# Performance work log

Measured on AMD Instinct MI355X. Metric: run time of the kernel, lower is better.

## Reference

```python
import jax, jax.numpy as jnp
import numpy as np

EMBED_DIM = 512
NUM_HEADS = 8
HEAD_DIM = EMBED_DIM // NUM_HEADS  # 64
ROT_T = 32  # head_dim * rope_fraction // 2
ROT_V = 32
ROPE_BASE = 10000.0


def _rope_cos_sin(idx, rot_dim, base=ROPE_BASE):
    # idx: (S,) int positions -> cos,sin: (S, rot_dim//2)
    half = rot_dim // 2
    inv_freq = 1.0 / (base ** (jnp.arange(half, dtype=jnp.float32) / half))
    angles = idx.astype(jnp.float32)[:, None] * inv_freq[None, :]  # (S, half)
    return jnp.cos(angles), jnp.sin(angles)


def _apply_rope(x, cos, sin):
    # x: (B,H,S,R) with R even; cos/sin: (S, R//2)
    xe = x[..., ::2]
    xo = x[..., 1::2]
    c = cos[None, None]  # (1,1,S,R//2)
    s = sin[None, None]
    oe = xe * c - xo * s
    oo = xe * s + xo * c
    # re-interleave even/odd lanes
    return jnp.stack([oe, oo], axis=-1).reshape(x.shape)


def setup_inputs() -> dict:
    key = jax.random.key(0)
    ks = jax.random.split(key, 5)
    B, S, D = 2, 4096, EMBED_DIM
    scale_w = 1.0 / np.sqrt(D)
    return {
        "x": jax.random.normal(ks[0], (B, S, D), dtype=jnp.float32),
        "Wq": jax.random.normal(ks[1], (D, D), dtype=jnp.float32) * scale_w,
        "Wk": jax.random.normal(ks[2], (D, D), dtype=jnp.float32) * scale_w,
        "Wv": jax.random.normal(ks[3], (D, D), dtype=jnp.float32) * scale_w,
        "Wo": jax.random.normal(ks[4], (D, D), dtype=jnp.float32) * scale_w,
        "T": 128,
        "V": 32,
    }


def reference(x, Wq, Wk, Wv, Wo, T, V):
    B, S, D = x.shape
    H, hd = NUM_HEADS, HEAD_DIM
    scale = hd ** -0.5

    def split_heads(y):
        return y.reshape(B, S, H, hd).transpose(0, 2, 1, 3)  # (B,H,S,hd)

    q = split_heads(x @ Wq.T)
    k = split_heads(x @ Wk.T)
    v = split_heads(x @ Wv.T)

    p = jnp.arange(S)
    t_idx = p // V
    v_idx = p % V
    cos_t, sin_t = _rope_cos_sin(t_idx, ROT_T)
    cos_v, sin_v = _rope_cos_sin(v_idx, ROT_V)

    te, ve = ROT_T, ROT_T + ROT_V
    q = jnp.concatenate([
        _apply_rope(q[..., :te], cos_t, sin_t),
        _apply_rope(q[..., te:ve], cos_v, sin_v),
        q[..., ve:],
    ], axis=-1)
    k = jnp.concatenate([
        _apply_rope(k[..., :te], cos_t, sin_t),
        _apply_rope(k[..., te:ve], cos_v, sin_v),
        k[..., ve:],
    ], axis=-1)

    attn = jnp.einsum("bhqd,bhkd->bhqk", q, k) * scale  # (B,H,S,S)
    attn = jax.nn.softmax(attn, axis=-1)
    y = jnp.einsum("bhqk,bhkd->bhqd", attn, v)
    y = y.transpose(0, 2, 1, 3).reshape(B, S, D)
    return y @ Wo.T
```

## Files before the change

kernel.cpp:

```cpp
#include <hip/hip_runtime.h>
#include <hip/hip_bf16.h>

#define SEQ 4096
#define BSZ 2
#define NH 8
#define HD 64
#define DMODEL 512

typedef __bf16 bf16_t;
typedef __bf16 bf16x8 __attribute__((ext_vector_type(8)));
typedef __bf16 bf16x4 __attribute__((ext_vector_type(4)));
typedef float f32x4 __attribute__((ext_vector_type(4)));

__device__ __forceinline__ f32x4 mfma16(bf16x8 a, bf16x8 b, f32x4 c) {
    return __builtin_amdgcn_mfma_f32_16x16x32_bf16(a, b, c, 0, 0, 0);
}

__device__ __forceinline__ bf16x8 ld8(const bf16_t* p) {
    return *reinterpret_cast<const bf16x8*>(p);
}

__device__ __forceinline__ uint32_t pack2(bf16_t a, bf16_t b) {
    union { bf16_t h[2]; uint32_t u; } x;
    x.h[0] = a; x.h[1] = b;
    return x.u;
}

__device__ __forceinline__ void gl_lds16(const bf16_t* g, bf16_t* l) {
    __builtin_amdgcn_global_load_lds(
        (const __attribute__((address_space(1))) uint32_t*)g,
        (__attribute__((address_space(3))) uint32_t*)l,
        16, 0, 0);
}

__global__ void cast_all(const float* __restrict__ x,
                         const float* __restrict__ wq, const float* __restrict__ wk,
                         const float* __restrict__ wv, const float* __restrict__ wo,
                         bf16_t* __restrict__ Xb, bf16_t* __restrict__ Wc,
                         bf16_t* __restrict__ Wob) {
    int i = blockIdx.x * blockDim.x + threadIdx.x;
    const float* src;
    bf16_t* dst;
    int j;
    if (i < 1048576) { src = x; dst = Xb; j = i; }
    else {
        int k = i - 1048576;
        int w = k >> 16;
        j = k & 65535;
        src = (w == 0) ? wq : (w == 1) ? wk : (w == 2) ? wv : wo;
        dst = (w == 3) ? Wob : Wc + w * 262144;
    }
    float4 v = reinterpret_cast<const float4*>(src)[j];
    bf16x4 o;
    o[0] = (bf16_t)v.x; o[1] = (bf16_t)v.y; o[2] = (bf16_t)v.z; o[3] = (bf16_t)v.w;
    reinterpret_cast<bf16x4*>(dst)[j] = o;
}

__global__ __launch_bounds__(256) void gemm_qkv(const bf16_t* __restrict__ A,
                                                const bf16_t* __restrict__ W,
                                                bf16_t* __restrict__ Qb,
                                                bf16_t* __restrict__ Kb,
                                                bf16_t* __restrict__ Vb,
                                                const int* __restrict__ Vpar) {
    __shared__ bf16_t As[2 * 128 * 32];
    __shared__ bf16_t Bs[2 * 128 * 32];
    const int lane = threadIdx.x & 63;
    const int wid = threadIdx.x >> 6;
    const int c = lane & 15, quad = lane >> 4;
    const int wm = wid & 1, wn = wid >> 1;
    const int m0 = blockIdx.x * 128;
    const int n0 = blockIdx.y * 128;

    f32x4 acc[4][4];
#pragma unroll
    for (int i = 0; i < 4; i++)
#pragma unroll
        for (int j = 0; j < 4; j++) acc[i][j] = f32x4{0.f, 0.f, 0.f, 0.f};

    const int lrow = lane >> 2;
    const int lch = lane & 3;
    const bf16_t* Ag = A + (size_t)(m0 + wid * 32 + lrow) * 512 + lch * 8;
    const bf16_t* Bg = W + (size_t)(n0 + wid * 32 + lrow) * 512 + lch * 8;
    const int w0 = (wid * 32) * 32;
    const int w1 = (wid * 32 + 16) * 32;

    gl_lds16(Ag, As + w0);
    gl_lds16(Ag + 16 * 512, As + w1);
    gl_lds16(Bg, Bs + w0);
    gl_lds16(Bg + 16 * 512, Bs + w1);

    for (int it = 0; it < 16; it++) {
        __syncthreads();

        if (it + 1 < 16) {
            int k0 = (it + 1) * 32;
            int bo = ((it + 1) & 1) * 4096;
            gl_lds16(Ag + k0, As + bo + w0);
            gl_lds16(Ag + 16 * 512 + k0, As + bo + w1);
            gl_lds16(Bg + k0, Bs + bo + w0);
            gl_lds16(Bg + 16 * 512 + k0, Bs + bo + w1);
        }

        const bf16_t* Ab = As + (it & 1) * 4096;
        const bf16_t* Bb = Bs + (it & 1) * 4096;
        bf16x8 a[4], b[4];
#pragma unroll
        for (int i = 0; i < 4; i++) a[i] = ld8(&Ab[(wm * 64 + i * 16 + c) * 32 + quad * 8]);
#pragma unroll
        for (int j = 0; j < 4; j++) b[j] = ld8(&Bb[(wn * 64 + j * 16 + c) * 32 + quad * 8]);
#pragma unroll
        for (int i = 0; i < 4; i++)
#pragma unroll
            for (int j = 0; j < 4; j++) acc[i][j] = mfma16(a[i], b[j], acc[i][j]);
    }

    const int Vv = Vpar[0];
    const float qs = 0.1803368801111204f;
    const bool codd = (c & 1);

#pragma unroll
    for (int i = 0; i < 4; i++) {
        int mbase = m0 + wm * 64 + i * 16 + quad * 4;
#pragma unroll
        for (int j = 0; j < 4; j++) {
            int col = n0 + wn * 64 + j * 16 + c;
            int which = col >> 9;
            int h = (col >> 6) & 7;
            int d = col & 63;
            f32x4 v = acc[i][j];
            if (which < 2) {
                int fidx = (d & 31) >> 1;
                float inv = exp2f((float)fidx * -0.8304820237218407f);
                bool hi = (d >= 32);
                f32x4 part;
#pragma unroll
                for (int r = 0; r < 4; r++) part[r] = __shfl_xor(v[r], 1, 64);
#pragma unroll
                for (int r = 0; r < 4; r++) {
                    int s = (mbase + r) & 4095;
                    int tq = s / Vv;
                    int vq = s - tq * Vv;
                    float ang = (float)(hi ? vq : tq) * inv;
                    float sn = __sinf(ang), cs = __cosf(ang);
                    float xe = codd ? part[r] : v[r];
                    float xo = codd ? v[r] : part[r];
                    v[r] = codd ? (xe * sn + xo * cs) : (xe * cs - xo * sn);
                }
                if (which == 0) {
#pragma unroll
                    for (int r = 0; r < 4; r++) v[r] *= qs;
                }
            }
            bf16_t* dst = (which == 0) ? Qb : ((which == 1) ? Kb : Vb);

            float p0 = __shfl_xor(v[0], 1, 64);
            float p1 = __shfl_xor(v[1], 1, 64);
            float p2 = __shfl_xor(v[2], 1, 64);
            float p3 = __shfl_xor(v[3], 1, 64);
            uint32_t u0 = codd ? pack2((bf16_t)p2, (bf16_t)v[2])
                               : pack2((bf16_t)v[0], (bf16_t)p0);
            uint32_t u1 = codd ? pack2((bf16_t)p3, (bf16_t)v[3])
                               : pack2((bf16_t)v[1], (bf16_t)p1);
            int dcol = d & ~1;
            int m = mbase + (codd ? 2 : 0);
            {
                int b_ = m >> 12, s = m & 4095;
                *(uint32_t*)&dst[((size_t)(b_ * NH + h) * SEQ + s) * HD + dcol] = u0;
                m++;
                b_ = m >> 12; s = m & 4095;
                *(uint32_t*)&dst[((size_t)(b_ * NH + h) * SEQ + s) * HD + dcol] = u1;
            }
        }
    }
}

__global__ __launch_bounds__(256) void gemm_out(const bf16_t* __restrict__ A,
                                                const bf16_t* __restrict__ W,
                                                float* __restrict__ out) {
    __shared__ bf16_t As[2 * 128 * 32];
    __shared__ bf16_t Bs[2 * 64 * 32];
    const int t = threadIdx.x;
    const int lane = t & 63;
    const int wid = t >> 6;
    const int c = lane & 15, quad = lane >> 4;
    const int m0 = blockIdx.x * 128;
    const int n0 = blockIdx.y * 64;

    f32x4 acc[2][4];
#pragma unroll
    for (int i = 0; i < 2; i++)
#pragma unroll
        for (int j = 0; j < 4; j++) acc[i][j] = f32x4{0.f, 0.f, 0.f, 0.f};

    const int lrow = lane >> 2;
    const int lch = lane & 3;
    const bf16_t* Ag = A + (size_t)(m0 + wid * 32 + lrow) * 512 + lch * 8;
    const bf16_t* Bg = W + (size_t)(n0 + wid * 16 + lrow) * 512 + lch * 8;
    const int aw0 = (wid * 32) * 32;
    const int aw1 = (wid * 32 + 16) * 32;
    const int bw = (wid * 16) * 32;

    gl_lds16(Ag, As + aw0);
    gl_lds16(Ag + 16 * 512, As + aw1);
    gl_lds16(Bg, Bs + bw);

    for (int it = 0; it < 16; it++) {
        __syncthreads();

        if (it + 1 < 16) {
            int k0 = (it + 1) * 32;
            int ao = ((it + 1) & 1) * 4096;
            int bo = ((it + 1) & 1) * 2048;
            gl_lds16(Ag + k0, As + ao + aw0);
            gl_lds16(Ag + 16 * 512 + k0, As + ao + aw1);
            gl_lds16(Bg + k0, Bs + bo + bw);
        }

        const bf16_t* Ab = As + (it & 1) * 4096;
        const bf16_t* Bb = Bs + (it & 1) * 2048;
        bf16x8 a[2], b[4];
#pragma unroll
        for (int i = 0; i < 2; i++) a[i] = ld8(&Ab[(wid * 32 + i * 16 + c) * 32 + quad * 8]);
#pragma unroll
        for (int j = 0; j < 4; j++) b[j] = ld8(&Bb[(j * 16 + c) * 32 + quad * 8]);
#pragma unroll
        for (int i = 0; i < 2; i++)
#pragma unroll
            for (int j = 0; j < 4; j++) acc[i][j] = mfma16(a[i], b[j], acc[i][j]);
    }

#pragma unroll
    for (int i = 0; i < 2; i++) {
        int mbase = m0 + wid * 32 + i * 16 + quad * 4;
#pragma unroll
        for (int j = 0; j < 4; j++) {
            int col = n0 + j * 16 + c;
#pragma unroll
            for (int r = 0; r < 4; r++)
                out[(size_t)(mbase + r) * DMODEL + col] = acc[i][j][r];
        }
    }
}

__global__ __launch_bounds__(256, 2) void flash_attn(const bf16_t* __restrict__ Q,
                                                     const bf16_t* __restrict__ K,
                                                     const bf16_t* __restrict__ V,
                                                     bf16_t* __restrict__ Y) {
    __shared__ __align__(16) unsigned char smem[65536];

    const int t = threadIdx.x;
    const int lane = t & 63;
    const int c = lane & 15, quad = lane >> 4;
    const int wid = t >> 6;
    const int w = wid & 1;
    const int pr = wid >> 1;
    const int bh = blockIdx.x & 15;
    const int qx = blockIdx.x >> 4;
    const int qw = qx * 128 + w * 64;

    size_t base = (size_t)bh * SEQ * HD;
    const bf16_t* Qp = Q + base;
    const bf16_t* Vp = V + base + (size_t)pr * 2048 * HD;

    unsigned char* pairBase = smem + pr * 32768;

    const bf16_t* Kpb = K + base + (size_t)pr * 2048 * HD;
    int srcOff = w * 4096 + ((lane >> 3) * 128) +
                 (((lane & 7) ^ ((lane >> 3) & 3)) * 16);
    const bf16_t* kE = (const bf16_t*)((const unsigned char*)Kpb + srcOff);
    const bf16_t* kO = (const bf16_t*)((const unsigned char*)Kpb + (srcOff ^ 64));

    bf16x8 qf[4][2];
#pragma unroll
    for (int qt = 0; qt < 4; qt++)
#pragma unroll
        for (int ks = 0; ks < 2; ks++)
            qf[qt][ks] = ld8(Qp + (size_t)(qw + qt * 16 + c) * HD + ks * 32 + quad * 8);

    f32x4 acc[4][4];
#pragma unroll
    for (int qt = 0; qt < 4; qt++)
#pragma unroll
        for (int dt = 0; dt < 4; dt++) acc[qt][dt] = f32x4{0.f, 0.f, 0.f, 0.f};
    float lsum[4] = {0.f, 0.f, 0.f, 0.f};

    const int tp = t & 127;
    const int kva = 2 * (tp & 31);
    const int dc = 16 * (tp >> 5);

    {
        bf16_t* dst = (bf16_t*)(pairBase + w * 4096);
#pragma unroll
        for (int i = 0; i < 4; i++)
            gl_lds16(((i & 1) ? kO : kE) + i * 512, dst + i * 512);
        kE += 4096; kO += 4096;
    }
    bf16x8 vr0 = ld8(Vp + (size_t)kva * HD + dc);
    bf16x8 vr1 = ld8(Vp + (size_t)(kva + 1) * HD + dc);
    bf16x8 vr2 = ld8(Vp + (size_t)kva * HD + dc + 8);
    bf16x8 vr3 = ld8(Vp + (size_t)(kva + 1) * HD + dc + 8);

    for (int kt = 0; kt < 32; kt++) {
        uint32_t* vt = (uint32_t*)(pairBase + 16384 + (kt & 1) * 8192);

#pragma unroll
        for (int j = 0; j < 8; j++) {
            int d0 = dc + j;
            int sv0 = (d0 & 7) ^ ((d0 >> 3) & 7);
            vt[d0 * 32 + (((kva >> 3) ^ sv0) & 7) * 4 + ((kva & 6) >> 1)] = pack2(vr0[j], vr1[j]);
            int d1 = dc + 8 + j;
            int sv1 = (d1 & 7) ^ ((d1 >> 3) & 7);
            vt[d1 * 32 + (((kva >> 3) ^ sv1) & 7) * 4 + ((kva & 6) >> 1)] = pack2(vr2[j], vr3[j]);
        }

        __syncthreads();

        if (kt + 1 < 32) {
            bf16_t* dst = (bf16_t*)(pairBase + ((kt + 1) & 1) * 8192 + w * 4096);
#pragma unroll
            for (int i = 0; i < 4; i++)
                gl_lds16(((i & 1) ? kO : kE) + i * 512, dst + i * 512);
            kE += 4096; kO += 4096;
            int kv0n = (kt + 1) * 64;
            vr0 = ld8(Vp + (size_t)(kv0n + kva) * HD + dc);
            vr1 = ld8(Vp + (size_t)(kv0n + kva + 1) * HD + dc);
            vr2 = ld8(Vp + (size_t)(kv0n + kva) * HD + dc + 8);
            vr3 = ld8(Vp + (size_t)(kv0n + kva + 1) * HD + dc + 8);
        }

        const uint4* kl = (const uint4*)(pairBase + (kt & 1) * 8192);

        f32x4 st[4][4];
#pragma unroll
        for (int n = 0; n < 4; n++) {
            int kvr = (n >> 1) * 32 + ((c >> 2) * 8) + ((n & 1) * 4) + (c & 3);
            int sk = (kvr & 3) | (((kvr >> 3) & 1) << 2);
            bf16x8 k0 = *reinterpret_cast<const bf16x8*>(&kl[kvr * 8 + (quad ^ sk)]);
            bf16x8 k1 = *reinterpret_cast<const bf16x8*>(&kl[kvr * 8 + ((4 + quad) ^ sk)]);
#pragma unroll
            for (int qt = 0; qt < 4; qt++) {
                f32x4 z = f32x4{0.f, 0.f, 0.f, 0.f};
                z = mfma16(k0, qf[qt][0], z);
                z = mfma16(k1, qf[qt][1], z);
                st[qt][n] = z;
            }
        }

        bf16x8 pf[4][2];
#pragma unroll
        for (int qt = 0; qt < 4; qt++) {
            float e[4][4];
            float ls = 0.f;
#pragma unroll
            for (int n = 0; n < 4; n++)
#pragma unroll
                for (int r = 0; r < 4; r++) {
                    float v = __builtin_amdgcn_exp2f(st[qt][n][r]);
                    e[n][r] = v;
                    ls += v;
                }
            lsum[qt] += ls;
            bf16x8 f0, f1;
#pragma unroll
            for (int j = 0; j < 8; j++) {
                f0[j] = (bf16_t)e[(j >> 2)][j & 3];
                f1[j] = (bf16_t)e[2 + (j >> 2)][j & 3];
            }
            pf[qt][0] = f0;
            pf[qt][1] = f1;
        }

#pragma unroll
        for (int dt = 0; dt < 4; dt++) {
            int d = dt * 16 + c;
            int sv = (d & 7) ^ ((d >> 3) & 7);
            bf16x8 v0f = *reinterpret_cast<const bf16x8*>(&vt[d * 32 + ((quad ^ sv) & 7) * 4]);
            bf16x8 v1f = *reinterpret_cast<const bf16x8*>(&vt[d * 32 + (((4 + quad) ^ sv) & 7) * 4]);
#pragma unroll
            for (int qt = 0; qt < 4; qt++) {
                acc[qt][dt] = mfma16(v0f, pf[qt][0], acc[qt][dt]);
                acc[qt][dt] = mfma16(v1f, pf[qt][1], acc[qt][dt]);
            }
        }
    }

    float lred[4];
#pragma unroll
    for (int qt = 0; qt < 4; qt++) {
        float lt = lsum[qt];
        lt += __shfl_xor(lt, 16, 64);
        lt += __shfl_xor(lt, 32, 64);
        lred[qt] = lt;
    }

    __syncthreads();
    float* Ox = (float*)smem;
    float* Lx = (float*)(smem + 128 * 68 * 4);

    if (pr == 1) {
#pragma unroll
        for (int qt = 0; qt < 4; qt++) {
            int ql = w * 64 + qt * 16 + c;
#pragma unroll
            for (int dt = 0; dt < 4; dt++)
                *reinterpret_cast<f32x4*>(&Ox[ql * 68 + dt * 16 + quad * 4]) = acc[qt][dt];
            if (quad == 0) Lx[ql] = lred[qt];
        }
    }
    __syncthreads();
    if (pr == 0) {
        int b_ = bh >> 3, h = bh & 7;
#pragma unroll
        for (int qt = 0; qt < 4; qt++) {
            int ql = w * 64 + qt * 16 + c;
            float inv_l = 1.0f / (lred[qt] + Lx[ql]);
            int srow = qw + qt * 16 + c;
            bf16_t* yrow = Y + (size_t)(b_ * SEQ + srow) * DMODEL + h * HD;
#pragma unroll
            for (int dt = 0; dt < 4; dt++) {
                f32x4 o4 = acc[qt][dt] + *reinterpret_cast<const f32x4*>(&Ox[ql * 68 + dt * 16 + quad * 4]);
                bf16x4 o;
#pragma unroll
                for (int r = 0; r < 4; r++) o[r] = (bf16_t)(o4[r] * inv_l);
                *reinterpret_cast<bf16x4*>(yrow + dt * 16 + quad * 4) = o;
            }
        }
    }
}

extern "C" void kernel_launch(void* const* d_in, const int* in_sizes, int n_in,
                              void* d_out, int out_size, void* d_ws, size_t ws_size,
                              hipStream_t stream) {
    (void)in_sizes; (void)n_in; (void)out_size; (void)ws_size;
    const float* x  = (const float*)d_in[0];
    const float* Wq = (const float*)d_in[1];
    const float* Wk = (const float*)d_in[2];
    const float* Wv = (const float*)d_in[3];
    const float* Wo = (const float*)d_in[4];
    const int*   Vp = (const int*)d_in[6];
    float* out = (float*)d_out;

    bf16_t* ws  = (bf16_t*)d_ws;
    bf16_t* Xb  = ws;
    bf16_t* Wc  = Xb  + 4194304;
    bf16_t* Wob = Wc  + 786432;
    bf16_t* Qb  = Wob + 262144;
    bf16_t* Kb  = Qb  + 4194304;
    bf16_t* Vb  = Kb  + 4194304;
    bf16_t* Yb  = Vb  + 4194304;

    cast_all<<<5120, 256, 0, stream>>>(x, Wq, Wk, Wv, Wo, Xb, Wc, Wob);

    gemm_qkv<<<dim3(64, 12), 256, 0, stream>>>(Xb, Wc, Qb, Kb, Vb, Vp);

    flash_attn<<<512, 256, 0, stream>>>(Qb, Kb, Vb, Yb);

    gemm_out<<<dim3(64, 8), 256, 0, stream>>>(Yb, Wob, out);
}
```

Before: 205.9 us.

## Fuse fp32-to-bf16 cast of x into QKV GEMM A-tile loads

```diff
diff --git a/kernel.cpp b/kernel.cpp
--- a/kernel.cpp
+++ b/kernel.cpp
@@ -33,30 +33,20 @@
         16, 0, 0);
 }
 
-__global__ void cast_all(const float* __restrict__ x,
-                         const float* __restrict__ wq, const float* __restrict__ wk,
-                         const float* __restrict__ wv, const float* __restrict__ wo,
-                         bf16_t* __restrict__ Xb, bf16_t* __restrict__ Wc,
-                         bf16_t* __restrict__ Wob) {
+__global__ void cast_w(const float* __restrict__ wq, const float* __restrict__ wk,
+                       const float* __restrict__ wv, const float* __restrict__ wo,
+                       bf16_t* __restrict__ Wc, bf16_t* __restrict__ Wob) {
     int i = blockIdx.x * blockDim.x + threadIdx.x;
-    const float* src;
-    bf16_t* dst;
-    int j;
-    if (i < 1048576) { src = x; dst = Xb; j = i; }
-    else {
-        int k = i - 1048576;
-        int w = k >> 16;
-        j = k & 65535;
-        src = (w == 0) ? wq : (w == 1) ? wk : (w == 2) ? wv : wo;
-        dst = (w == 3) ? Wob : Wc + w * 262144;
-    }
+    int w = i >> 16, j = i & 65535;
+    const float* src = (w == 0) ? wq : (w == 1) ? wk : (w == 2) ? wv : wo;
+    bf16_t* dst = (w == 3) ? Wob : Wc + w * 262144;
     float4 v = reinterpret_cast<const float4*>(src)[j];
     bf16x4 o;
     o[0] = (bf16_t)v.x; o[1] = (bf16_t)v.y; o[2] = (bf16_t)v.z; o[3] = (bf16_t)v.w;
     reinterpret_cast<bf16x4*>(dst)[j] = o;
 }
 
-__global__ __launch_bounds__(256) void gemm_qkv(const bf16_t* __restrict__ A,
+__global__ __launch_bounds__(256) void gemm_qkv(const float* __restrict__ A,
                                                 const bf16_t* __restrict__ W,
                                                 bf16_t* __restrict__ Qb,
                                                 bf16_t* __restrict__ Kb,
@@ -79,26 +69,40 @@
 
     const int lrow = lane >> 2;
     const int lch = lane & 3;
-    const bf16_t* Ag = A + (size_t)(m0 + wid * 32 + lrow) * 512 + lch * 8;
     const bf16_t* Bg = W + (size_t)(n0 + wid * 32 + lrow) * 512 + lch * 8;
     const int w0 = (wid * 32) * 32;
     const int w1 = (wid * 32 + 16) * 32;
 
-    gl_lds16(Ag, As + w0);
-    gl_lds16(Ag + 16 * 512, As + w1);
+    const float* Ag32 = A + (size_t)(m0 + wid * 32 + (lane >> 3)) * 512 + (lane & 7) * 4;
+    bf16_t* Aw = As + (wid * 32 + (lane >> 3)) * 32 + (lane & 7) * 4;
+
+    float4 ar[4];
+#pragma unroll
+    for (int i = 0; i < 4; i++)
+        ar[i] = *reinterpret_cast<const float4*>(Ag32 + (size_t)i * 8 * 512);
     gl_lds16(Bg, Bs + w0);
     gl_lds16(Bg + 16 * 512, Bs + w1);
 
     for (int it = 0; it < 16; it++) {
+        bf16_t* aw = Aw + (it & 1) * 4096;
+#pragma unroll
+        for (int i = 0; i < 4; i++) {
+            bf16x4 c4;
+            c4[0] = (bf16_t)ar[i].x; c4[1] = (bf16_t)ar[i].y;
+            c4[2] = (bf16_t)ar[i].z; c4[3] = (bf16_t)ar[i].w;
+            *reinterpret_cast<bf16x4*>(aw + i * 8 * 32) = c4;
+        }
+
         __syncthreads();
 
         if (it + 1 < 16) {
             int k0 = (it + 1) * 32;
             int bo = ((it + 1) & 1) * 4096;
-            gl_lds16(Ag + k0, As + bo + w0);
-            gl_lds16(Ag + 16 * 512 + k0, As + bo + w1);
             gl_lds16(Bg + k0, Bs + bo + w0);
             gl_lds16(Bg + 16 * 512 + k0, Bs + bo + w1);
+#pragma unroll
+            for (int i = 0; i < 4; i++)
+                ar[i] = *reinterpret_cast<const float4*>(Ag32 + (size_t)i * 8 * 512 + k0);
         }
 
         const bf16_t* Ab = As + (it & 1) * 4096;
@@ -441,17 +445,16 @@
     float* out = (float*)d_out;
 
     bf16_t* ws  = (bf16_t*)d_ws;
-    bf16_t* Xb  = ws;
-    bf16_t* Wc  = Xb  + 4194304;
+    bf16_t* Wc  = ws;
     bf16_t* Wob = Wc  + 786432;
     bf16_t* Qb  = Wob + 262144;
     bf16_t* Kb  = Qb  + 4194304;
     bf16_t* Vb  = Kb  + 4194304;
     bf16_t* Yb  = Vb  + 4194304;
 
-    cast_all<<<5120, 256, 0, stream>>>(x, Wq, Wk, Wv, Wo, Xb, Wc, Wob);
-
-    gemm_qkv<<<dim3(64, 12), 256, 0, stream>>>(Xb, Wc, Qb, Kb, Vb, Vp);
+    cast_w<<<1024, 256, 0, stream>>>(Wq, Wk, Wv, Wo, Wc, Wob);
+
+    gemm_qkv<<<dim3(64, 12), 256, 0, stream>>>(x, Wc, Qb, Kb, Vb, Vp);
 
     flash_attn<<<512, 256, 0, stream>>>(Qb, Kb, Vb, Yb);
 
```

Result: no change. 203.8 us (-1.0%).
